# Optimization experiments

Hardware: AMD Instinct MI355X
Metric: run time of the kernel (lower is better)

Reference implementation:

```python
import jax, jax.numpy as jnp
import numpy as np

D_MODEL = 1024
NUM_HEADS = 16
D_K = D_MODEL // NUM_HEADS


def setup_inputs() -> dict:
    key = jax.random.key(0)
    ks = jax.random.split(key, 9)
    B, S = 2, 2048
    s = 1.0 / np.sqrt(D_MODEL)
    return {
        "x": jax.random.normal(ks[0], (B, S, D_MODEL), dtype=jnp.float32),
        "Wq": jax.random.normal(ks[1], (D_MODEL, D_MODEL), dtype=jnp.float32) * s,
        "bq": jnp.zeros((D_MODEL,), dtype=jnp.float32),
        "Wk": jax.random.normal(ks[2], (D_MODEL, D_MODEL), dtype=jnp.float32) * s,
        "bk": jnp.zeros((D_MODEL,), dtype=jnp.float32),
        "Wv": jax.random.normal(ks[3], (D_MODEL, D_MODEL), dtype=jnp.float32) * s,
        "bv": jnp.zeros((D_MODEL,), dtype=jnp.float32),
        "Wo": jax.random.normal(ks[4], (D_MODEL, D_MODEL), dtype=jnp.float32) * s,
        "bo": jnp.zeros((D_MODEL,), dtype=jnp.float32),
    }


def reference(x, Wq, bq, Wk, bk, Wv, bv, Wo, bo):
    B, S, _ = x.shape
    # project and split heads: [B, H, S, d_k]
    def proj(W, b):
        return (x @ W + b).reshape(B, S, NUM_HEADS, D_K).transpose(0, 2, 1, 3)
    Q, K, V = proj(Wq, bq), proj(Wk, bk), proj(Wv, bv)
    scores = jnp.einsum("bhqd,bhkd->bhqk", Q, K) / jnp.sqrt(jnp.float32(D_K))
    causal = jnp.tril(jnp.ones((S, S), dtype=bool))
    scores = jnp.where(causal[None, None], scores, jnp.float32(-1e9))
    attn = jax.nn.softmax(scores, axis=-1)  # dropout=0 (eval)
    out = jnp.einsum("bhqk,bhkd->bhqd", attn, V)
    out = out.transpose(0, 2, 1, 3).reshape(B, S, D_MODEL)
    return out @ Wo + bo
```

## Files before the change

kernel.cpp:

```cpp
#include <hip/hip_runtime.h>

#define SEQ    2048
#define NH     16
#define DMODEL 1024

typedef __attribute__((ext_vector_type(4))) float f32x4;
typedef __attribute__((ext_vector_type(8))) short s16x8;
typedef __attribute__((ext_vector_type(4))) short s16x4;

__device__ __forceinline__ float bf2f(unsigned short u){
  union { unsigned int i; float f; } v; v.i = ((unsigned int)u) << 16; return v.f;
}
__device__ __forceinline__ unsigned short f2bf(float f){
  union { float f; unsigned int i; } v; v.f = f;
  unsigned int r = v.i + 0x7fffu + ((v.i >> 16) & 1u);
  return (unsigned short)(r >> 16);
}
__device__ __forceinline__ unsigned short f2bf_hu(float f){
  union { float f; unsigned int i; } v; v.f = f;
  return (unsigned short)((v.i + 0x8000u) >> 16);
}
__device__ __forceinline__ float fast_exp2(float x){
  return __builtin_amdgcn_exp2f(x);
}
__device__ __forceinline__ void gld_lds16(const void* g, void* l){
  __builtin_amdgcn_global_load_lds((const __attribute__((address_space(1))) void*)g,
                                   (__attribute__((address_space(3))) void*)l,
                                   16, 0, 0);
}

__global__ __launch_bounds__(256) void k_cast_x(const float* __restrict__ x,
                                                unsigned short* __restrict__ hi){
  int i = blockIdx.x * 256 + threadIdx.x;
  f32x4 v = ((const f32x4*)x)[i];
  s16x4 h;
  #pragma unroll
  for (int j = 0; j < 4; ++j) h[j] = (short)f2bf(v[j]);
  ((s16x4*)hi)[i] = h;
}

__global__ __launch_bounds__(256) void k_t_w(const float* __restrict__ W0,
                                             const float* __restrict__ W1,
                                             const float* __restrict__ W2,
                                             const float* __restrict__ W3,
                                             unsigned short* __restrict__ Wt){
  __shared__ float t[64][65];
  const float* Ws[4] = {W0, W1, W2, W3};
  const float* W = Ws[blockIdx.z];
  const int n0 = blockIdx.x * 64, k0 = blockIdx.y * 64;
  const int tid = threadIdx.x;
  #pragma unroll
  for (int i = 0; i < 16; ++i){
    int e = i * 256 + tid;
    int r = e >> 6, c = e & 63;
    t[r][c] = W[(size_t)(k0 + r) * 1024 + n0 + c];
  }
  __syncthreads();
  size_t base = ((size_t)blockIdx.z << 20);
  #pragma unroll
  for (int i = 0; i < 16; ++i){
    int e = i * 256 + tid;
    int nn = e >> 6, kk = e & 63;
    Wt[base + (size_t)(n0 + nn) * 1024 + k0 + kk] = f2bf(t[kk][nn]);
  }
}

__global__ __launch_bounds__(256, 3)
void gemm_qkv(const unsigned short* __restrict__ A,
              const unsigned short* __restrict__ B,
              const float* __restrict__ bq, const float* __restrict__ bk,
              const float* __restrict__ bv,
              unsigned short* __restrict__ Qb, unsigned short* __restrict__ Kb,
              unsigned short* __restrict__ Vt)
{
  __shared__ __align__(16) unsigned short lA[2][128 * 32];
  __shared__ __align__(16) unsigned short lB[2][128 * 32];
  const int tid = threadIdx.x;
  const int lane = tid & 63, w = tid >> 6;
  const int wm = w >> 1, wn = w & 1;
  const int lr = lane & 15, lq = lane >> 4;
  const int m0 = blockIdx.y * 128, n0 = blockIdx.x * 128;

  auto stage = [&](int buf, int k0){
    #pragma unroll
    for (int it = 0; it < 2; ++it){
      int c = it * 256 + tid;
      int row = c >> 2, cc = c & 3;
      gld_lds16(A + (size_t)(m0 + row) * 1024 + k0 + cc * 8, &lA[buf][c * 8]);
      gld_lds16(B + (size_t)(n0 + row) * 1024 + k0 + cc * 8, &lB[buf][c * 8]);
    }
  };

  f32x4 acc[4][4];
  #pragma unroll
  for (int i = 0; i < 4; ++i)
    #pragma unroll
    for (int j = 0; j < 4; ++j) acc[i][j] = (f32x4)0.0f;

  stage(0, 0);
  __syncthreads();
  for (int k0 = 0; k0 < 1024; k0 += 32){
    const int cur = (k0 >> 5) & 1;
    if (k0 + 32 < 1024) stage(cur ^ 1, k0 + 32);
    s16x8 fa[4], fb[4];
    #pragma unroll
    for (int f = 0; f < 4; ++f){
      fa[f] = *(const s16x8*)&lA[cur][(wm * 64 + f * 16 + lr) * 32 + lq * 8];
      fb[f] = *(const s16x8*)&lB[cur][(wn * 64 + f * 16 + lr) * 32 + lq * 8];
    }
    #pragma unroll
    for (int i = 0; i < 4; ++i)
      #pragma unroll
      for (int j = 0; j < 4; ++j)
        acc[i][j] = __builtin_amdgcn_mfma_f32_16x16x32_bf16(fa[i], fb[j], acc[i][j], 0, 0, 0);
    __syncthreads();
  }

  const int mat = n0 >> 10;
  const float* bias = (mat == 0) ? bq : (mat == 1) ? bk : bv;
  unsigned short* QK = (mat == 0) ? Qb : Kb;
  const int mb = m0 + wm * 64, nb = n0 + wn * 64;
  #pragma unroll
  for (int i = 0; i < 4; ++i){
    int row = mb + i * 16 + lq * 4;
    #pragma unroll
    for (int j = 0; j < 4; ++j){
      int col = (nb + j * 16 + lr) & 1023;
      float bs = bias[col];
      if (mat < 2){
        #pragma unroll
        for (int r = 0; r < 4; ++r)
          QK[(size_t)(row + r) * 1024 + col] = f2bf(acc[i][j][r] + bs);
      } else {
        int bb = row >> 11, s = row & 2047;
        int h = col >> 6, d = col & 63;
        s16x4 pk;
        #pragma unroll
        for (int r = 0; r < 4; ++r) pk[r] = (short)f2bf(acc[i][j][r] + bs);
        *(s16x4*)&Vt[(((size_t)(bb * NH + h) * 64 + d) << 11) + s] = pk;
      }
    }
  }
}

__global__ __launch_bounds__(256, 2)
void gemm_o(const unsigned short* __restrict__ A,
            const unsigned short* __restrict__ B,
            const float* __restrict__ bias,
            float* __restrict__ C)
{
  __shared__ __align__(16) unsigned short lA[2][64 * 32];
  __shared__ __align__(16) unsigned short lB[2][128 * 32];
  const int tid = threadIdx.x;
  const int lane = tid & 63, w = tid >> 6;
  const int wm = w >> 1, wn = w & 1;
  const int lr = lane & 15, lq = lane >> 4;
  const int m0 = blockIdx.y * 64, n0 = blockIdx.x * 128;

  auto stage = [&](int buf, int k0){
    {
      int c = tid;
      int row = c >> 2, cc = c & 3;
      gld_lds16(A + (size_t)(m0 + row) * 1024 + k0 + cc * 8, &lA[buf][c * 8]);
    }
    #pragma unroll
    for (int it = 0; it < 2; ++it){
      int c = it * 256 + tid;
      int row = c >> 2, cc = c & 3;
      gld_lds16(B + (size_t)(n0 + row) * 1024 + k0 + cc * 8, &lB[buf][c * 8]);
    }
  };

  f32x4 acc[2][4];
  #pragma unroll
  for (int i = 0; i < 2; ++i)
    #pragma unroll
    for (int j = 0; j < 4; ++j) acc[i][j] = (f32x4)0.0f;

  stage(0, 0);
  __syncthreads();
  for (int k0 = 0; k0 < 1024; k0 += 32){
    const int cur = (k0 >> 5) & 1;
    if (k0 + 32 < 1024) stage(cur ^ 1, k0 + 32);
    s16x8 fa[2], fb[4];
    #pragma unroll
    for (int f = 0; f < 2; ++f)
      fa[f] = *(const s16x8*)&lA[cur][(wm * 32 + f * 16 + lr) * 32 + lq * 8];
    #pragma unroll
    for (int f = 0; f < 4; ++f)
      fb[f] = *(const s16x8*)&lB[cur][(wn * 64 + f * 16 + lr) * 32 + lq * 8];
    #pragma unroll
    for (int i = 0; i < 2; ++i)
      #pragma unroll
      for (int j = 0; j < 4; ++j)
        acc[i][j] = __builtin_amdgcn_mfma_f32_16x16x32_bf16(fa[i], fb[j], acc[i][j], 0, 0, 0);
    __syncthreads();
  }

  const int mb = m0 + wm * 32, nb = n0 + wn * 64;
  #pragma unroll
  for (int i = 0; i < 2; ++i){
    int row = mb + i * 16 + lq * 4;
    #pragma unroll
    for (int j = 0; j < 4; ++j){
      int col = nb + j * 16 + lr;
      float bs = bias[col];
      #pragma unroll
      for (int r = 0; r < 4; ++r)
        C[(size_t)(row + r) * 1024 + col] = acc[i][j][r] + bs;
    }
  }
}

__global__ __launch_bounds__(256, 4)
void attn_fwd(const unsigned short* __restrict__ Qg,
              const unsigned short* __restrict__ Kg,
              const unsigned short* __restrict__ Vtg,
              unsigned short* __restrict__ Oh)
{
  __shared__ __align__(16) unsigned short lK[2][64 * 64];
  __shared__ __align__(16) unsigned short lV[2][64 * 64];
  __shared__ __align__(16) unsigned short lP[4][16 * 64];
  const int tid = threadIdx.x;
  const int lane = tid & 63, w = tid >> 6;
  const int lr = lane & 15, lq = lane >> 4;
  const int bh = blockIdx.x;
  const int b = bh >> 4, h = bh & 15;
  const int qt = 31 - blockIdx.y;
  const int qrow = qt * 64 + w * 16;

  const float qscale = 0.125f * 1.44269504088896f;
  const float FIXMAX = 11.0f;

  const unsigned short* qp = Qg + (size_t)(b * SEQ + qrow + lr) * 1024 + h * 64 + lq * 8;
  s16x8 q0 = *(const s16x8*)qp;
  s16x8 q1 = *(const s16x8*)(qp + 32);
  #pragma unroll
  for (int j = 0; j < 8; ++j){
    q0[j] = (short)f2bf(bf2f((unsigned short)q0[j]) * qscale);
    q1[j] = (short)f2bf(bf2f((unsigned short)q1[j]) * qscale);
  }

  float ls[4];
  f32x4 accO[4];
  #pragma unroll
  for (int r = 0; r < 4; ++r){ ls[r] = 0.f; accO[r] = (f32x4)0.0f; }

  auto stage = [&](int buf, int kt){
    const int kc0 = kt * 64;
    #pragma unroll
    for (int it = 0; it < 2; ++it){
      int c = it * 256 + tid;
      int row = c >> 3, sc = c & 7;
      int lc = sc ^ (row & 7);
      gld_lds16(Kg + (size_t)(b * SEQ + kc0 + row) * 1024 + h * 64 + lc * 8, &lK[buf][c * 8]);
      gld_lds16(Vtg + ((size_t)(bh * 64 + row) << 11) + kc0 + lc * 8, &lV[buf][c * 8]);
    }
  };

  stage(0, 0);
  __syncthreads();
  for (int kt = 0; kt <= qt; ++kt){
    const int cur = kt & 1;
    if (kt < qt) stage(cur ^ 1, kt + 1);
    const bool diag = (kt == qt);

    f32x4 s4[4];
    #pragma unroll
    for (int st = 0; st < 4; ++st){
      if (diag && st > w){ s4[st] = (f32x4)(-1e30f); continue; }
      int tok = st * 16 + lr;
      const char* base = (const char*)&lK[cur][0] + tok * 128;
      s16x8 kf0 = *(const s16x8*)(base + (((0 + lq) ^ (tok & 7)) << 4));
      s16x8 kf1 = *(const s16x8*)(base + (((4 + lq) ^ (tok & 7)) << 4));
      f32x4 z = (f32x4)0.0f;
      z = __builtin_amdgcn_mfma_f32_16x16x32_bf16(q0, kf0, z, 0, 0, 0);
      z = __builtin_amdgcn_mfma_f32_16x16x32_bf16(q1, kf1, z, 0, 0, 0);
      s4[st] = z;
    }
    if (diag){
      #pragma unroll
      for (int st = 0; st < 4; ++st)
        if (st == w)
          #pragma unroll
          for (int r = 0; r < 4; ++r)
            if (lr > lq * 4 + r) s4[st][r] = -1e30f;
    }

    char* pb = (char*)&lP[w][0];
    #pragma unroll
    for (int st = 0; st < 4; ++st)
      #pragma unroll
      for (int r = 0; r < 4; ++r){
        float p = fast_exp2(s4[st][r] - FIXMAX);
        ls[r] += p;
        int prow = lq * 4 + r;
        int byo = (prow * 128 + (st * 16 + lr) * 2) ^ ((prow & 7) << 4);
        *(unsigned short*)(pb + byo) = f2bf_hu(p);
      }
    asm volatile("s_waitcnt lgkmcnt(0)" ::: "memory");
    s16x8 pf0 = *(const s16x8*)(pb + (lr * 128 + (((0 + lq) ^ (lr & 7)) << 4)));
    s16x8 pf1 = *(const s16x8*)(pb + (lr * 128 + (((4 + lq) ^ (lr & 7)) << 4)));

    #pragma unroll
    for (int dt = 0; dt < 4; ++dt){
      int drow = dt * 16 + lr;
      const char* vb = (const char*)&lV[cur][0] + drow * 128;
      s16x8 vf0 = *(const s16x8*)(vb + (((0 + lq) ^ (drow & 7)) << 4));
      s16x8 vf1 = *(const s16x8*)(vb + (((4 + lq) ^ (drow & 7)) << 4));
      accO[dt] = __builtin_amdgcn_mfma_f32_16x16x32_bf16(pf0, vf0, accO[dt], 0, 0, 0);
      accO[dt] = __builtin_amdgcn_mfma_f32_16x16x32_bf16(pf1, vf1, accO[dt], 0, 0, 0);
    }
    __syncthreads();
  }

  #pragma unroll
  for (int r = 0; r < 4; ++r){
    float t = ls[r];
    t += __shfl_xor(t, 1);
    t += __shfl_xor(t, 2);
    t += __shfl_xor(t, 4);
    t += __shfl_xor(t, 8);
    float rn = 1.0f / t;
    #pragma unroll
    for (int dt = 0; dt < 4; ++dt){
      size_t off = (size_t)(b * SEQ + qrow + lq * 4 + r) * 1024 + h * 64 + dt * 16 + lr;
      Oh[off] = f2bf(accO[dt][r] * rn);
    }
  }
}

extern "C" void kernel_launch(void* const* d_in, const int* in_sizes, int n_in,
                              void* d_out, int out_size, void* d_ws, size_t ws_size,
                              hipStream_t stream){
  (void)in_sizes; (void)n_in; (void)out_size; (void)ws_size;
  const float* x  = (const float*)d_in[0];
  const float* Wq = (const float*)d_in[1];
  const float* bq = (const float*)d_in[2];
  const float* Wk = (const float*)d_in[3];
  const float* bk = (const float*)d_in[4];
  const float* Wv = (const float*)d_in[5];
  const float* bv = (const float*)d_in[6];
  const float* Wo = (const float*)d_in[7];
  const float* bo = (const float*)d_in[8];

  const size_t NT = 4096;
  unsigned short* xh  = (unsigned short*)d_ws;
  unsigned short* wt  = xh + NT * 1024;
  unsigned short* Qb  = wt + 4u * 1024 * 1024;
  unsigned short* Kb  = Qb + NT * 1024;
  unsigned short* Vt  = Kb + NT * 1024;
  unsigned short* Ohb = Vt + NT * 1024;

  k_cast_x<<<4096, 256, 0, stream>>>(x, xh);
  k_t_w<<<dim3(16, 16, 4), 256, 0, stream>>>(Wq, Wk, Wv, Wo, wt);

  gemm_qkv<<<dim3(24, 32), 256, 0, stream>>>(xh, wt, bq, bk, bv, Qb, Kb, Vt);

  attn_fwd<<<dim3(32, 32), 256, 0, stream>>>(Qb, Kb, Vt, Ohb);

  const size_t WM = (size_t)1024 * 1024;
  gemm_o<<<dim3(8, 64), 256, 0, stream>>>(Ohb, wt + 3 * WM, bo, (float*)d_out);
}
```

Measured before the change: 115.3 us.

## Switch attention to 32x32x16 MFMA with transposed S and register P exchange

Rewrites the attention kernel so each of two waves owns 32 query rows and uses 32x32x16 bf16 MFMAs. It computes S transposed (K as the A operand), so the exponentiated P stays in registers and is rearranged with cross-half lane shuffles instead of going through LDS. This removes the per-wave P LDS buffer and its store, wait and reload round trip, and halves the block to 128 threads. In exchange each thread issues twice as many staging loads, holds larger accumulators that raise register pressure, and fewer waves are resident per block to hide latency.

```diff
diff --git a/kernel.cpp b/kernel.cpp
--- a/kernel.cpp
+++ b/kernel.cpp
@@ -4,9 +4,10 @@
 #define NH     16
 #define DMODEL 1024
 
-typedef __attribute__((ext_vector_type(4))) float f32x4;
-typedef __attribute__((ext_vector_type(8))) short s16x8;
-typedef __attribute__((ext_vector_type(4))) short s16x4;
+typedef __attribute__((ext_vector_type(4)))  float f32x4;
+typedef __attribute__((ext_vector_type(16))) float f32x16;
+typedef __attribute__((ext_vector_type(8)))  short s16x8;
+typedef __attribute__((ext_vector_type(4)))  short s16x4;
 
 __device__ __forceinline__ float bf2f(unsigned short u){
   union { unsigned int i; float f; } v; v.i = ((unsigned int)u) << 16; return v.f;
@@ -15,10 +16,6 @@
   union { float f; unsigned int i; } v; v.f = f;
   unsigned int r = v.i + 0x7fffu + ((v.i >> 16) & 1u);
   return (unsigned short)(r >> 16);
-}
-__device__ __forceinline__ unsigned short f2bf_hu(float f){
-  union { float f; unsigned int i; } v; v.f = f;
-  return (unsigned short)((v.i + 0x8000u) >> 16);
 }
 __device__ __forceinline__ float fast_exp2(float x){
   return __builtin_amdgcn_exp2f(x);
@@ -212,7 +209,7 @@
   }
 }
 
-__global__ __launch_bounds__(256, 4)
+__global__ __launch_bounds__(128, 2)
 void attn_fwd(const unsigned short* __restrict__ Qg,
               const unsigned short* __restrict__ Kg,
               const unsigned short* __restrict__ Vtg,
@@ -220,37 +217,38 @@
 {
   __shared__ __align__(16) unsigned short lK[2][64 * 64];
   __shared__ __align__(16) unsigned short lV[2][64 * 64];
-  __shared__ __align__(16) unsigned short lP[4][16 * 64];
   const int tid = threadIdx.x;
   const int lane = tid & 63, w = tid >> 6;
-  const int lr = lane & 15, lq = lane >> 4;
+  const int l31 = lane & 31, lh = lane >> 5;
   const int bh = blockIdx.x;
   const int b = bh >> 4, h = bh & 15;
   const int qt = 31 - blockIdx.y;
-  const int qrow = qt * 64 + w * 16;
+  const int qbase = qt * 64 + w * 32;
 
   const float qscale = 0.125f * 1.44269504088896f;
   const float FIXMAX = 11.0f;
 
-  const unsigned short* qp = Qg + (size_t)(b * SEQ + qrow + lr) * 1024 + h * 64 + lq * 8;
-  s16x8 q0 = *(const s16x8*)qp;
-  s16x8 q1 = *(const s16x8*)(qp + 32);
-  #pragma unroll
-  for (int j = 0; j < 8; ++j){
-    q0[j] = (short)f2bf(bf2f((unsigned short)q0[j]) * qscale);
-    q1[j] = (short)f2bf(bf2f((unsigned short)q1[j]) * qscale);
-  }
-
-  float ls[4];
-  f32x4 accO[4];
-  #pragma unroll
-  for (int r = 0; r < 4; ++r){ ls[r] = 0.f; accO[r] = (f32x4)0.0f; }
+  s16x8 qf[4];
+  {
+    const unsigned short* qp = Qg + (size_t)(b * SEQ + qbase + l31) * 1024 + h * 64 + lh * 8;
+    #pragma unroll
+    for (int f = 0; f < 4; ++f){
+      s16x8 v = *(const s16x8*)(qp + f * 16);
+      #pragma unroll
+      for (int j = 0; j < 8; ++j)
+        v[j] = (short)f2bf(bf2f((unsigned short)v[j]) * qscale);
+      qf[f] = v;
+    }
+  }
+
+  float ls = 0.f;
+  f32x16 accO0 = (f32x16)0.0f, accO1 = (f32x16)0.0f;
 
   auto stage = [&](int buf, int kt){
     const int kc0 = kt * 64;
     #pragma unroll
-    for (int it = 0; it < 2; ++it){
-      int c = it * 256 + tid;
+    for (int it = 0; it < 4; ++it){
+      int c = it * 128 + tid;
       int row = c >> 3, sc = c & 7;
       int lc = sc ^ (row & 7);
       gld_lds16(Kg + (size_t)(b * SEQ + kc0 + row) * 1024 + h * 64 + lc * 8, &lK[buf][c * 8]);
@@ -265,68 +263,74 @@
     if (kt < qt) stage(cur ^ 1, kt + 1);
     const bool diag = (kt == qt);
 
-    f32x4 s4[4];
-    #pragma unroll
-    for (int st = 0; st < 4; ++st){
-      if (diag && st > w){ s4[st] = (f32x4)(-1e30f); continue; }
-      int tok = st * 16 + lr;
-      const char* base = (const char*)&lK[cur][0] + tok * 128;
-      s16x8 kf0 = *(const s16x8*)(base + (((0 + lq) ^ (tok & 7)) << 4));
-      s16x8 kf1 = *(const s16x8*)(base + (((4 + lq) ^ (tok & 7)) << 4));
-      f32x4 z = (f32x4)0.0f;
-      z = __builtin_amdgcn_mfma_f32_16x16x32_bf16(q0, kf0, z, 0, 0, 0);
-      z = __builtin_amdgcn_mfma_f32_16x16x32_bf16(q1, kf1, z, 0, 0, 0);
-      s4[st] = z;
-    }
-    if (diag){
-      #pragma unroll
-      for (int st = 0; st < 4; ++st)
-        if (st == w)
-          #pragma unroll
-          for (int r = 0; r < 4; ++r)
-            if (lr > lq * 4 + r) s4[st][r] = -1e30f;
-    }
-
-    char* pb = (char*)&lP[w][0];
-    #pragma unroll
-    for (int st = 0; st < 4; ++st)
-      #pragma unroll
-      for (int r = 0; r < 4; ++r){
-        float p = fast_exp2(s4[st][r] - FIXMAX);
-        ls[r] += p;
-        int prow = lq * 4 + r;
-        int byo = (prow * 128 + (st * 16 + lr) * 2) ^ ((prow & 7) << 4);
-        *(unsigned short*)(pb + byo) = f2bf_hu(p);
+    #pragma unroll
+    for (int s = 0; s < 2; ++s){
+      if (!(diag && s > w)){
+        f32x16 p = (f32x16)0.0f;
+        #pragma unroll
+        for (int f = 0; f < 4; ++f){
+          int row = s * 32 + l31;
+          int ch = ((f * 2 + lh) ^ (row & 7)) << 4;
+          s16x8 kf = *(const s16x8*)((const char*)&lK[cur][0] + row * 128 + ch);
+          p = __builtin_amdgcn_mfma_f32_32x32x16_bf16(kf, qf[f], p, 0, 0, 0);
+        }
+        const bool pmask = diag && (s == w);
+        float pe[16];
+        #pragma unroll
+        for (int i = 0; i < 16; ++i){
+          float sv = p[i];
+          if (pmask && ((i & 3) + 8 * (i >> 2) + 4 * lh > l31)) sv = -1e30f;
+          float e = fast_exp2(sv - FIXMAX);
+          pe[i] = e;
+          ls += e;
+        }
+        unsigned c0 = ((unsigned)f2bf(pe[1])  << 16) | f2bf(pe[0]);
+        unsigned c1 = ((unsigned)f2bf(pe[3])  << 16) | f2bf(pe[2]);
+        unsigned c2 = ((unsigned)f2bf(pe[5])  << 16) | f2bf(pe[4]);
+        unsigned c3 = ((unsigned)f2bf(pe[7])  << 16) | f2bf(pe[6]);
+        unsigned c4 = ((unsigned)f2bf(pe[9])  << 16) | f2bf(pe[8]);
+        unsigned c5 = ((unsigned)f2bf(pe[11]) << 16) | f2bf(pe[10]);
+        unsigned c6 = ((unsigned)f2bf(pe[13]) << 16) | f2bf(pe[12]);
+        unsigned c7 = ((unsigned)f2bf(pe[15]) << 16) | f2bf(pe[14]);
+        unsigned xc0 = __shfl_xor(c0, 32), xc1 = __shfl_xor(c1, 32);
+        unsigned xc2 = __shfl_xor(c2, 32), xc3 = __shfl_xor(c3, 32);
+        unsigned xc4 = __shfl_xor(c4, 32), xc5 = __shfl_xor(c5, 32);
+        unsigned xc6 = __shfl_xor(c6, 32), xc7 = __shfl_xor(c7, 32);
+        union { unsigned u[4]; s16x8 v; } pa0, pa1;
+        pa0.u[0] = lh ? xc2 : c0;  pa0.u[1] = lh ? xc3 : c1;
+        pa0.u[2] = lh ? c2 : xc0;  pa0.u[3] = lh ? c3 : xc1;
+        pa1.u[0] = lh ? xc6 : c4;  pa1.u[1] = lh ? xc7 : c5;
+        pa1.u[2] = lh ? c6 : xc4;  pa1.u[3] = lh ? c7 : xc5;
+
+        #pragma unroll
+        for (int kh = 0; kh < 2; ++kh){
+          s16x8 pa = kh ? pa1.v : pa0.v;
+          {
+            int row = l31;
+            int ch = ((s * 4 + kh * 2 + lh) ^ (row & 7)) << 4;
+            s16x8 vf = *(const s16x8*)((const char*)&lV[cur][0] + row * 128 + ch);
+            accO0 = __builtin_amdgcn_mfma_f32_32x32x16_bf16(pa, vf, accO0, 0, 0, 0);
+          }
+          {
+            int row = 32 + l31;
+            int ch = ((s * 4 + kh * 2 + lh) ^ (row & 7)) << 4;
+            s16x8 vf = *(const s16x8*)((const char*)&lV[cur][0] + row * 128 + ch);
+            accO1 = __builtin_amdgcn_mfma_f32_32x32x16_bf16(pa, vf, accO1, 0, 0, 0);
+          }
+        }
       }
-    asm volatile("s_waitcnt lgkmcnt(0)" ::: "memory");
-    s16x8 pf0 = *(const s16x8*)(pb + (lr * 128 + (((0 + lq) ^ (lr & 7)) << 4)));
-    s16x8 pf1 = *(const s16x8*)(pb + (lr * 128 + (((4 + lq) ^ (lr & 7)) << 4)));
-
-    #pragma unroll
-    for (int dt = 0; dt < 4; ++dt){
-      int drow = dt * 16 + lr;
-      const char* vb = (const char*)&lV[cur][0] + drow * 128;
-      s16x8 vf0 = *(const s16x8*)(vb + (((0 + lq) ^ (drow & 7)) << 4));
-      s16x8 vf1 = *(const s16x8*)(vb + (((4 + lq) ^ (drow & 7)) << 4));
-      accO[dt] = __builtin_amdgcn_mfma_f32_16x16x32_bf16(pf0, vf0, accO[dt], 0, 0, 0);
-      accO[dt] = __builtin_amdgcn_mfma_f32_16x16x32_bf16(pf1, vf1, accO[dt], 0, 0, 0);
     }
     __syncthreads();
   }
 
-  #pragma unroll
-  for (int r = 0; r < 4; ++r){
-    float t = ls[r];
-    t += __shfl_xor(t, 1);
-    t += __shfl_xor(t, 2);
-    t += __shfl_xor(t, 4);
-    t += __shfl_xor(t, 8);
-    float rn = 1.0f / t;
-    #pragma unroll
-    for (int dt = 0; dt < 4; ++dt){
-      size_t off = (size_t)(b * SEQ + qrow + lq * 4 + r) * 1024 + h * 64 + dt * 16 + lr;
-      Oh[off] = f2bf(accO[dt][r] * rn);
-    }
+  ls += __shfl_xor(ls, 32);
+  #pragma unroll
+  for (int i = 0; i < 16; ++i){
+    int qloc = (i & 3) + 8 * (i >> 2) + 4 * lh;
+    float rn = 1.0f / __shfl(ls, qloc);
+    size_t off = (size_t)(b * SEQ + qbase + qloc) * 1024 + h * 64 + l31;
+    Oh[off]      = f2bf(accO0[i] * rn);
+    Oh[off + 32] = f2bf(accO1[i] * rn);
   }
 }
 
@@ -357,7 +361,7 @@
 
   gemm_qkv<<<dim3(24, 32), 256, 0, stream>>>(xh, wt, bq, bk, bv, Qb, Kb, Vt);
 
-  attn_fwd<<<dim3(32, 32), 256, 0, stream>>>(Qb, Kb, Vt, Ohb);
+  attn_fwd<<<dim3(32, 32), 128, 0, stream>>>(Qb, Kb, Vt, Ohb);
 
   const size_t WM = (size_t)1024 * 1024;
   gemm_o<<<dim3(8, 64), 256, 0, stream>>>(Ohb, wt + 3 * WM, bo, (float*)d_out);
```

Result: slower. 128.5 us (+11.5%).

## Give each attention wave two query groups to reuse K/V fragments

Applied to the files above, without the earlier changes.

The attention kernel now runs 128 threads (2 waves) per block, and each wave handles two 16-row query groups. K and V fragments are loaded from LDS into registers once per tile and reused for both groups, which halves LDS fragment reads per query row. The QK^T product is computed transposed (K as the A operand), so the P writes can be packed 32-bit stores and the row sums are reduced across lanes differently. In exchange each wave holds more registers, and there are fewer waves per block to hide latency.

```diff
diff --git a/kernel.cpp b/kernel.cpp
--- a/kernel.cpp
+++ b/kernel.cpp
@@ -4,9 +4,9 @@
 #define NH     16
 #define DMODEL 1024
 
-typedef __attribute__((ext_vector_type(4))) float f32x4;
-typedef __attribute__((ext_vector_type(8))) short s16x8;
-typedef __attribute__((ext_vector_type(4))) short s16x4;
+typedef __attribute__((ext_vector_type(4)))  float f32x4;
+typedef __attribute__((ext_vector_type(8)))  short s16x8;
+typedef __attribute__((ext_vector_type(4)))  short s16x4;
 
 __device__ __forceinline__ float bf2f(unsigned short u){
   union { unsigned int i; float f; } v; v.i = ((unsigned int)u) << 16; return v.f;
@@ -212,7 +212,7 @@
   }
 }
 
-__global__ __launch_bounds__(256, 4)
+__global__ __launch_bounds__(128, 2)
 void attn_fwd(const unsigned short* __restrict__ Qg,
               const unsigned short* __restrict__ Kg,
               const unsigned short* __restrict__ Vtg,
@@ -220,37 +220,44 @@
 {
   __shared__ __align__(16) unsigned short lK[2][64 * 64];
   __shared__ __align__(16) unsigned short lV[2][64 * 64];
-  __shared__ __align__(16) unsigned short lP[4][16 * 64];
+  __shared__ __align__(16) unsigned short lP[2][16 * 64];
   const int tid = threadIdx.x;
   const int lane = tid & 63, w = tid >> 6;
   const int lr = lane & 15, lq = lane >> 4;
   const int bh = blockIdx.x;
   const int b = bh >> 4, h = bh & 15;
   const int qt = 31 - blockIdx.y;
-  const int qrow = qt * 64 + w * 16;
 
   const float qscale = 0.125f * 1.44269504088896f;
   const float FIXMAX = 11.0f;
 
-  const unsigned short* qp = Qg + (size_t)(b * SEQ + qrow + lr) * 1024 + h * 64 + lq * 8;
-  s16x8 q0 = *(const s16x8*)qp;
-  s16x8 q1 = *(const s16x8*)(qp + 32);
-  #pragma unroll
-  for (int j = 0; j < 8; ++j){
-    q0[j] = (short)f2bf(bf2f((unsigned short)q0[j]) * qscale);
-    q1[j] = (short)f2bf(bf2f((unsigned short)q1[j]) * qscale);
-  }
-
-  float ls[4];
-  f32x4 accO[4];
-  #pragma unroll
-  for (int r = 0; r < 4; ++r){ ls[r] = 0.f; accO[r] = (f32x4)0.0f; }
+  s16x8 qf[2][2];
+  #pragma unroll
+  for (int g = 0; g < 2; ++g){
+    const int qrow = qt * 64 + (w * 2 + g) * 16;
+    const unsigned short* qp = Qg + (size_t)(b * SEQ + qrow + lr) * 1024 + h * 64 + lq * 8;
+    s16x8 v0 = *(const s16x8*)qp;
+    s16x8 v1 = *(const s16x8*)(qp + 32);
+    #pragma unroll
+    for (int j = 0; j < 8; ++j){
+      v0[j] = (short)f2bf(bf2f((unsigned short)v0[j]) * qscale);
+      v1[j] = (short)f2bf(bf2f((unsigned short)v1[j]) * qscale);
+    }
+    qf[g][0] = v0; qf[g][1] = v1;
+  }
+
+  float ls[2] = {0.f, 0.f};
+  f32x4 accO[2][4];
+  #pragma unroll
+  for (int g = 0; g < 2; ++g)
+    #pragma unroll
+    for (int dt = 0; dt < 4; ++dt) accO[g][dt] = (f32x4)0.0f;
 
   auto stage = [&](int buf, int kt){
     const int kc0 = kt * 64;
     #pragma unroll
-    for (int it = 0; it < 2; ++it){
-      int c = it * 256 + tid;
+    for (int it = 0; it < 4; ++it){
+      int c = it * 128 + tid;
       int row = c >> 3, sc = c & 7;
       int lc = sc ^ (row & 7);
       gld_lds16(Kg + (size_t)(b * SEQ + kc0 + row) * 1024 + h * 64 + lc * 8, &lK[buf][c * 8]);
@@ -265,67 +272,80 @@
     if (kt < qt) stage(cur ^ 1, kt + 1);
     const bool diag = (kt == qt);
 
-    f32x4 s4[4];
+    s16x8 kf[4][2];
     #pragma unroll
     for (int st = 0; st < 4; ++st){
-      if (diag && st > w){ s4[st] = (f32x4)(-1e30f); continue; }
       int tok = st * 16 + lr;
-      const char* base = (const char*)&lK[cur][0] + tok * 128;
-      s16x8 kf0 = *(const s16x8*)(base + (((0 + lq) ^ (tok & 7)) << 4));
-      s16x8 kf1 = *(const s16x8*)(base + (((4 + lq) ^ (tok & 7)) << 4));
-      f32x4 z = (f32x4)0.0f;
-      z = __builtin_amdgcn_mfma_f32_16x16x32_bf16(q0, kf0, z, 0, 0, 0);
-      z = __builtin_amdgcn_mfma_f32_16x16x32_bf16(q1, kf1, z, 0, 0, 0);
-      s4[st] = z;
-    }
-    if (diag){
-      #pragma unroll
-      for (int st = 0; st < 4; ++st)
-        if (st == w)
-          #pragma unroll
-          for (int r = 0; r < 4; ++r)
-            if (lr > lq * 4 + r) s4[st][r] = -1e30f;
-    }
-
-    char* pb = (char*)&lP[w][0];
-    #pragma unroll
-    for (int st = 0; st < 4; ++st)
-      #pragma unroll
-      for (int r = 0; r < 4; ++r){
-        float p = fast_exp2(s4[st][r] - FIXMAX);
-        ls[r] += p;
-        int prow = lq * 4 + r;
-        int byo = (prow * 128 + (st * 16 + lr) * 2) ^ ((prow & 7) << 4);
-        *(unsigned short*)(pb + byo) = f2bf_hu(p);
-      }
-    asm volatile("s_waitcnt lgkmcnt(0)" ::: "memory");
-    s16x8 pf0 = *(const s16x8*)(pb + (lr * 128 + (((0 + lq) ^ (lr & 7)) << 4)));
-    s16x8 pf1 = *(const s16x8*)(pb + (lr * 128 + (((4 + lq) ^ (lr & 7)) << 4)));
-
+      const char* kb = (const char*)&lK[cur][0] + tok * 128;
+      kf[st][0] = *(const s16x8*)(kb + (((0 + lq) ^ (tok & 7)) << 4));
+      kf[st][1] = *(const s16x8*)(kb + (((4 + lq) ^ (tok & 7)) << 4));
+    }
+    s16x8 vf[4][2];
     #pragma unroll
     for (int dt = 0; dt < 4; ++dt){
       int drow = dt * 16 + lr;
       const char* vb = (const char*)&lV[cur][0] + drow * 128;
-      s16x8 vf0 = *(const s16x8*)(vb + (((0 + lq) ^ (drow & 7)) << 4));
-      s16x8 vf1 = *(const s16x8*)(vb + (((4 + lq) ^ (drow & 7)) << 4));
-      accO[dt] = __builtin_amdgcn_mfma_f32_16x16x32_bf16(pf0, vf0, accO[dt], 0, 0, 0);
-      accO[dt] = __builtin_amdgcn_mfma_f32_16x16x32_bf16(pf1, vf1, accO[dt], 0, 0, 0);
+      vf[dt][0] = *(const s16x8*)(vb + (((0 + lq) ^ (drow & 7)) << 4));
+      vf[dt][1] = *(const s16x8*)(vb + (((4 + lq) ^ (drow & 7)) << 4));
+    }
+
+    #pragma unroll
+    for (int g = 0; g < 2; ++g){
+      const int sg = w * 2 + g;
+      f32x4 s4[4];
+      #pragma unroll
+      for (int st = 0; st < 4; ++st){
+        if (diag && st > sg){ s4[st] = (f32x4)(-1e30f); continue; }
+        f32x4 z = (f32x4)0.0f;
+        z = __builtin_amdgcn_mfma_f32_16x16x32_bf16(kf[st][0], qf[g][0], z, 0, 0, 0);
+        z = __builtin_amdgcn_mfma_f32_16x16x32_bf16(kf[st][1], qf[g][1], z, 0, 0, 0);
+        if (diag && st == sg){
+          #pragma unroll
+          for (int r = 0; r < 4; ++r)
+            if (lq * 4 + r > lr) z[r] = -1e30f;
+        }
+        s4[st] = z;
+      }
+      char* pb = (char*)&lP[w][0];
+      #pragma unroll
+      for (int st = 0; st < 4; ++st){
+        float p0 = fast_exp2(s4[st][0] - FIXMAX);
+        float p1 = fast_exp2(s4[st][1] - FIXMAX);
+        float p2 = fast_exp2(s4[st][2] - FIXMAX);
+        float p3 = fast_exp2(s4[st][3] - FIXMAX);
+        ls[g] += (p0 + p1) + (p2 + p3);
+        unsigned d0 = ((unsigned)f2bf_hu(p1) << 16) | f2bf_hu(p0);
+        unsigned d1 = ((unsigned)f2bf_hu(p3) << 16) | f2bf_hu(p2);
+        int base = lr * 128 + ((st * 32 + lq * 8) ^ ((lr & 7) << 4));
+        *(unsigned*)(pb + base)     = d0;
+        *(unsigned*)(pb + base + 4) = d1;
+      }
+      asm volatile("s_waitcnt lgkmcnt(0)" ::: "memory");
+      s16x8 pf0 = *(const s16x8*)(pb + lr * 128 + ((((0 + lq) << 4)) ^ ((lr & 7) << 4)));
+      s16x8 pf1 = *(const s16x8*)(pb + lr * 128 + ((((4 + lq) << 4)) ^ ((lr & 7) << 4)));
+      #pragma unroll
+      for (int dt = 0; dt < 4; ++dt){
+        accO[g][dt] = __builtin_amdgcn_mfma_f32_16x16x32_bf16(pf0, vf[dt][0], accO[g][dt], 0, 0, 0);
+        accO[g][dt] = __builtin_amdgcn_mfma_f32_16x16x32_bf16(pf1, vf[dt][1], accO[g][dt], 0, 0, 0);
+      }
     }
     __syncthreads();
   }
 
   #pragma unroll
-  for (int r = 0; r < 4; ++r){
-    float t = ls[r];
-    t += __shfl_xor(t, 1);
-    t += __shfl_xor(t, 2);
-    t += __shfl_xor(t, 4);
-    t += __shfl_xor(t, 8);
-    float rn = 1.0f / t;
-    #pragma unroll
-    for (int dt = 0; dt < 4; ++dt){
-      size_t off = (size_t)(b * SEQ + qrow + lq * 4 + r) * 1024 + h * 64 + dt * 16 + lr;
-      Oh[off] = f2bf(accO[dt][r] * rn);
+  for (int g = 0; g < 2; ++g){
+    float t = ls[g];
+    t += __shfl_xor(t, 16);
+    t += __shfl_xor(t, 32);
+    const int qrow = qt * 64 + (w * 2 + g) * 16;
+    #pragma unroll
+    for (int r = 0; r < 4; ++r){
+      float rn = 1.0f / __shfl(t, lq * 4 + r);
+      #pragma unroll
+      for (int dt = 0; dt < 4; ++dt){
+        size_t off = (size_t)(b * SEQ + qrow + lq * 4 + r) * 1024 + h * 64 + dt * 16 + lr;
+        Oh[off] = f2bf(accO[g][dt][r] * rn);
+      }
     }
   }
 }
@@ -357,7 +377,7 @@
 
   gemm_qkv<<<dim3(24, 32), 256, 0, stream>>>(xh, wt, bq, bk, bv, Qb, Kb, Vt);
 
-  attn_fwd<<<dim3(32, 32), 256, 0, stream>>>(Qb, Kb, Vt, Ohb);
+  attn_fwd<<<dim3(32, 32), 128, 0, stream>>>(Qb, Kb, Vt, Ohb);
 
   const size_t WM = (size_t)1024 * 1024;
   gemm_o<<<dim3(8, 64), 256, 0, stream>>>(Ohb, wt + 3 * WM, bo, (float*)d_out);
```

Result: slower. 120.3 us (+4.3%).

## Transpose QK^T MFMA operands for packed P stores; shrink output GEMM tile

Applied to the files above, without the earlier changes.

In the attention kernel the score MFMA operands are swapped so each lane holds four consecutive key columns of one query row. That lets P be written to LDS as one packed 8-byte store per subtile instead of sixteen 2-byte stores. The row-sum becomes a single scalar per lane, reduced with two shuffles and then broadcast. Separately, the output projection GEMM tile shrinks from 64x128 to 64x64 with doubled grid and higher occupancy bound, trading operand reuse for more blocks in flight.

```diff
diff --git a/kernel.cpp b/kernel.cpp
--- a/kernel.cpp
+++ b/kernel.cpp
@@ -4,9 +4,10 @@
 #define NH     16
 #define DMODEL 1024
 
-typedef __attribute__((ext_vector_type(4))) float f32x4;
-typedef __attribute__((ext_vector_type(8))) short s16x8;
-typedef __attribute__((ext_vector_type(4))) short s16x4;
+typedef __attribute__((ext_vector_type(4)))  float f32x4;
+typedef __attribute__((ext_vector_type(8)))  short s16x8;
+typedef __attribute__((ext_vector_type(4)))  short s16x4;
+typedef __attribute__((ext_vector_type(2)))  unsigned u32x2;
 
 __device__ __forceinline__ float bf2f(unsigned short u){
   union { unsigned int i; float f; } v; v.i = ((unsigned int)u) << 16; return v.f;
@@ -143,66 +144,58 @@
   }
 }
 
-__global__ __launch_bounds__(256, 2)
+__global__ __launch_bounds__(256, 4)
 void gemm_o(const unsigned short* __restrict__ A,
             const unsigned short* __restrict__ B,
             const float* __restrict__ bias,
             float* __restrict__ C)
 {
   __shared__ __align__(16) unsigned short lA[2][64 * 32];
-  __shared__ __align__(16) unsigned short lB[2][128 * 32];
+  __shared__ __align__(16) unsigned short lB[2][64 * 32];
   const int tid = threadIdx.x;
   const int lane = tid & 63, w = tid >> 6;
   const int wm = w >> 1, wn = w & 1;
   const int lr = lane & 15, lq = lane >> 4;
-  const int m0 = blockIdx.y * 64, n0 = blockIdx.x * 128;
+  const int m0 = blockIdx.y * 64, n0 = blockIdx.x * 64;
 
   auto stage = [&](int buf, int k0){
-    {
-      int c = tid;
-      int row = c >> 2, cc = c & 3;
-      gld_lds16(A + (size_t)(m0 + row) * 1024 + k0 + cc * 8, &lA[buf][c * 8]);
-    }
-    #pragma unroll
-    for (int it = 0; it < 2; ++it){
-      int c = it * 256 + tid;
-      int row = c >> 2, cc = c & 3;
-      gld_lds16(B + (size_t)(n0 + row) * 1024 + k0 + cc * 8, &lB[buf][c * 8]);
-    }
+    int c = tid;
+    int row = c >> 2, cc = c & 3;
+    gld_lds16(A + (size_t)(m0 + row) * 1024 + k0 + cc * 8, &lA[buf][c * 8]);
+    gld_lds16(B + (size_t)(n0 + row) * 1024 + k0 + cc * 8, &lB[buf][c * 8]);
   };
 
-  f32x4 acc[2][4];
+  f32x4 acc[2][2];
   #pragma unroll
   for (int i = 0; i < 2; ++i)
     #pragma unroll
-    for (int j = 0; j < 4; ++j) acc[i][j] = (f32x4)0.0f;
+    for (int j = 0; j < 2; ++j) acc[i][j] = (f32x4)0.0f;
 
   stage(0, 0);
   __syncthreads();
   for (int k0 = 0; k0 < 1024; k0 += 32){
     const int cur = (k0 >> 5) & 1;
     if (k0 + 32 < 1024) stage(cur ^ 1, k0 + 32);
-    s16x8 fa[2], fb[4];
-    #pragma unroll
-    for (int f = 0; f < 2; ++f)
+    s16x8 fa[2], fb[2];
+    #pragma unroll
+    for (int f = 0; f < 2; ++f){
       fa[f] = *(const s16x8*)&lA[cur][(wm * 32 + f * 16 + lr) * 32 + lq * 8];
-    #pragma unroll
-    for (int f = 0; f < 4; ++f)
-      fb[f] = *(const s16x8*)&lB[cur][(wn * 64 + f * 16 + lr) * 32 + lq * 8];
+      fb[f] = *(const s16x8*)&lB[cur][(wn * 32 + f * 16 + lr) * 32 + lq * 8];
+    }
     #pragma unroll
     for (int i = 0; i < 2; ++i)
       #pragma unroll
-      for (int j = 0; j < 4; ++j)
+      for (int j = 0; j < 2; ++j)
         acc[i][j] = __builtin_amdgcn_mfma_f32_16x16x32_bf16(fa[i], fb[j], acc[i][j], 0, 0, 0);
     __syncthreads();
   }
 
-  const int mb = m0 + wm * 32, nb = n0 + wn * 64;
+  const int mb = m0 + wm * 32, nb = n0 + wn * 32;
   #pragma unroll
   for (int i = 0; i < 2; ++i){
     int row = mb + i * 16 + lq * 4;
     #pragma unroll
-    for (int j = 0; j < 4; ++j){
+    for (int j = 0; j < 2; ++j){
       int col = nb + j * 16 + lr;
       float bs = bias[col];
       #pragma unroll
@@ -241,10 +234,10 @@
     q1[j] = (short)f2bf(bf2f((unsigned short)q1[j]) * qscale);
   }
 
-  float ls[4];
+  float ls = 0.f;
   f32x4 accO[4];
   #pragma unroll
-  for (int r = 0; r < 4; ++r){ ls[r] = 0.f; accO[r] = (f32x4)0.0f; }
+  for (int dt = 0; dt < 4; ++dt) accO[dt] = (f32x4)0.0f;
 
   auto stage = [&](int buf, int kt){
     const int kc0 = kt * 64;
@@ -270,37 +263,37 @@
     for (int st = 0; st < 4; ++st){
       if (diag && st > w){ s4[st] = (f32x4)(-1e30f); continue; }
       int tok = st * 16 + lr;
-      const char* base = (const char*)&lK[cur][0] + tok * 128;
-      s16x8 kf0 = *(const s16x8*)(base + (((0 + lq) ^ (tok & 7)) << 4));
-      s16x8 kf1 = *(const s16x8*)(base + (((4 + lq) ^ (tok & 7)) << 4));
+      const char* kb = (const char*)&lK[cur][0] + tok * 128;
+      s16x8 kf0 = *(const s16x8*)(kb + (((0 + lq) ^ (tok & 7)) << 4));
+      s16x8 kf1 = *(const s16x8*)(kb + (((4 + lq) ^ (tok & 7)) << 4));
       f32x4 z = (f32x4)0.0f;
-      z = __builtin_amdgcn_mfma_f32_16x16x32_bf16(q0, kf0, z, 0, 0, 0);
-      z = __builtin_amdgcn_mfma_f32_16x16x32_bf16(q1, kf1, z, 0, 0, 0);
+      z = __builtin_amdgcn_mfma_f32_16x16x32_bf16(kf0, q0, z, 0, 0, 0);
+      z = __builtin_amdgcn_mfma_f32_16x16x32_bf16(kf1, q1, z, 0, 0, 0);
+      if (diag && st == w){
+        #pragma unroll
+        for (int r = 0; r < 4; ++r)
+          if (lq * 4 + r > lr) z[r] = -1e30f;
+      }
       s4[st] = z;
     }
-    if (diag){
-      #pragma unroll
-      for (int st = 0; st < 4; ++st)
-        if (st == w)
-          #pragma unroll
-          for (int r = 0; r < 4; ++r)
-            if (lr > lq * 4 + r) s4[st][r] = -1e30f;
-    }
 
     char* pb = (char*)&lP[w][0];
     #pragma unroll
-    for (int st = 0; st < 4; ++st)
-      #pragma unroll
-      for (int r = 0; r < 4; ++r){
-        float p = fast_exp2(s4[st][r] - FIXMAX);
-        ls[r] += p;
-        int prow = lq * 4 + r;
-        int byo = (prow * 128 + (st * 16 + lr) * 2) ^ ((prow & 7) << 4);
-        *(unsigned short*)(pb + byo) = f2bf_hu(p);
-      }
+    for (int st = 0; st < 4; ++st){
+      float p0 = fast_exp2(s4[st][0] - FIXMAX);
+      float p1 = fast_exp2(s4[st][1] - FIXMAX);
+      float p2 = fast_exp2(s4[st][2] - FIXMAX);
+      float p3 = fast_exp2(s4[st][3] - FIXMAX);
+      ls += (p0 + p1) + (p2 + p3);
+      u32x2 d;
+      d[0] = ((unsigned)f2bf_hu(p1) << 16) | f2bf_hu(p0);
+      d[1] = ((unsigned)f2bf_hu(p3) << 16) | f2bf_hu(p2);
+      int base = lr * 128 + ((st * 32 + lq * 8) ^ ((lr & 7) << 4));
+      *(u32x2*)(pb + base) = d;
+    }
     asm volatile("s_waitcnt lgkmcnt(0)" ::: "memory");
-    s16x8 pf0 = *(const s16x8*)(pb + (lr * 128 + (((0 + lq) ^ (lr & 7)) << 4)));
-    s16x8 pf1 = *(const s16x8*)(pb + (lr * 128 + (((4 + lq) ^ (lr & 7)) << 4)));
+    s16x8 pf0 = *(const s16x8*)(pb + lr * 128 + (((0 + lq) << 4) ^ ((lr & 7) << 4)));
+    s16x8 pf1 = *(const s16x8*)(pb + lr * 128 + (((4 + lq) << 4) ^ ((lr & 7) << 4)));
 
     #pragma unroll
     for (int dt = 0; dt < 4; ++dt){
@@ -314,14 +307,12 @@
     __syncthreads();
   }
 
+  float t = ls;
+  t += __shfl_xor(t, 16);
+  t += __shfl_xor(t, 32);
   #pragma unroll
   for (int r = 0; r < 4; ++r){
-    float t = ls[r];
-    t += __shfl_xor(t, 1);
-    t += __shfl_xor(t, 2);
-    t += __shfl_xor(t, 4);
-    t += __shfl_xor(t, 8);
-    float rn = 1.0f / t;
+    float rn = 1.0f / __shfl(t, lq * 4 + r);
     #pragma unroll
     for (int dt = 0; dt < 4; ++dt){
       size_t off = (size_t)(b * SEQ + qrow + lq * 4 + r) * 1024 + h * 64 + dt * 16 + lr;
@@ -360,5 +351,5 @@
   attn_fwd<<<dim3(32, 32), 256, 0, stream>>>(Qb, Kb, Vt, Ohb);
 
   const size_t WM = (size_t)1024 * 1024;
-  gemm_o<<<dim3(8, 64), 256, 0, stream>>>(Ohb, wt + 3 * WM, bo, (float*)d_out);
-}
+  gemm_o<<<dim3(16, 64), 256, 0, stream>>>(Ohb, wt + 3 * WM, bo, (float*)d_out);
+}
```

After: 113.8 us. About the same (-1.2%).
